# Kernel optimization log

Measured on AMD Instinct MI355X. Metric: run time of the kernel, lower is better.

The kernel has to match this reference:

```python
import jax, jax.numpy as jnp
import numpy as np

N = 50000      # nodes
E = 800000     # edges (before self loops)
H = 2          # attention heads
CH = 64        # per-head hidden channels
IN = 128       # input features
OUT = 64       # output channels
EPS = 1e-5     # batchnorm eps
SLOPE = 0.2    # LeakyReLU negative slope


def _gat_conv(x, src, dst, W, a_src, a_dst, b, concat):
    # x: [N, Fin]; W: [Fin, H*C]; a_src/a_dst: [H, C]
    n = x.shape[0]
    h = (x @ W).reshape(n, H, -1)                       # [N, H, C]
    al_s = (h * a_src).sum(-1)                          # [N, H]
    al_d = (h * a_dst).sum(-1)                          # [N, H]
    e = al_s[src] + al_d[dst]                           # [E, H]
    e = jnp.where(e > 0, e, SLOPE * e)                  # LeakyReLU
    # softmax over edges grouped by destination node
    m = jax.ops.segment_max(e, dst, num_segments=n)
    ex = jnp.exp(e - m[dst])
    den = jax.ops.segment_sum(ex, dst, num_segments=n)
    alpha = ex / (den[dst] + 1e-16)                     # [E, H]
    out = jax.ops.segment_sum(h[src] * alpha[:, :, None], dst, num_segments=n)
    out = out.reshape(n, -1) if concat else out.mean(axis=1)
    return out + b


def _batchnorm(x, g, be):
    mu = x.mean(axis=0)
    var = x.var(axis=0)  # biased, as torch BN uses in training
    return (x - mu) * jax.lax.rsqrt(var + EPS) * g + be


def setup_inputs() -> dict:
    key = jax.random.key(0)
    ks = jax.random.split(key, 18)
    s = 0.1
    inp = {
        "x": jax.random.normal(ks[0], (N, IN), jnp.float32),
        "edge_index": jax.random.randint(ks[1], (2, E), 0, N, jnp.int64),
        # layer 0: IN -> H*CH (concat)
        "W0": jax.random.normal(ks[2], (IN, H * CH), jnp.float32) * s,
        "a_src0": jax.random.normal(ks[3], (H, CH), jnp.float32) * s,
        "a_dst0": jax.random.normal(ks[4], (H, CH), jnp.float32) * s,
        "b0": jnp.zeros((H * CH,), jnp.float32),
        "g0": jnp.ones((H * CH,), jnp.float32),
        "be0": jnp.zeros((H * CH,), jnp.float32),
        # layer 1: H*CH -> H*CH (concat)
        "W1": jax.random.normal(ks[5], (H * CH, H * CH), jnp.float32) * s,
        "a_src1": jax.random.normal(ks[6], (H, CH), jnp.float32) * s,
        "a_dst1": jax.random.normal(ks[7], (H, CH), jnp.float32) * s,
        "b1": jnp.zeros((H * CH,), jnp.float32),
        "g1": jnp.ones((H * CH,), jnp.float32),
        "be1": jnp.zeros((H * CH,), jnp.float32),
        # layer 2: H*CH -> OUT, concat=False (mean over heads)
        "W2": jax.random.normal(ks[8], (H * CH, H * OUT), jnp.float32) * s,
        "a_src2": jax.random.normal(ks[9], (H, OUT), jnp.float32) * s,
        "a_dst2": jax.random.normal(ks[10], (H, OUT), jnp.float32) * s,
        "b2": jnp.zeros((OUT,), jnp.float32),
    }
    return inp


def reference(x, edge_index, W0, a_src0, a_dst0, b0, g0, be0,
              W1, a_src1, a_dst1, b1, g1, be1,
              W2, a_src2, a_dst2, b2):
    # add self loops (PyG GATConv default)
    loop = jnp.arange(N, dtype=edge_index.dtype)
    src = jnp.concatenate([edge_index[0], loop])
    dst = jnp.concatenate([edge_index[1], loop])

    h = _gat_conv(x, src, dst, W0, a_src0, a_dst0, b0, concat=True)
    h = jax.nn.relu(_batchnorm(h, g0, be0))
    # dropout: eval mode (identity)
    h = _gat_conv(h, src, dst, W1, a_src1, a_dst1, b1, concat=True)
    h = jax.nn.relu(_batchnorm(h, g1, be1))
    out = _gat_conv(h, src, dst, W2, a_src2, a_dst2, b2, concat=False)
    return out
```

## Files before the change

### kernel.cpp

```cpp
#include <hip/hip_runtime.h>


#define N_NODES 50000
#define N_EDGES 800000
#define ET (N_EDGES + N_NODES)
#define FDIM 128
#define SLOPE 0.2f
#define BN_EPS 1e-5f
#define SCAN_NB 196

typedef __attribute__((ext_vector_type(8))) short bf16x8;
typedef __attribute__((ext_vector_type(4))) float f32x4;
typedef __attribute__((ext_vector_type(8))) unsigned short u16x8;

__device__ __forceinline__ unsigned short f2bf(float f) {
  unsigned u = __float_as_uint(f);
  u = u + 0x7fffu + ((u >> 16) & 1u);
  return (unsigned short)(u >> 16);
}
__device__ __forceinline__ float bflo(unsigned p) { return __uint_as_float(p << 16); }
__device__ __forceinline__ float bfhi(unsigned p) { return __uint_as_float(p & 0xffff0000u); }


__global__ __launch_bounds__(256) void hist_rank(const int* __restrict__ dst,
                                                 int* __restrict__ counts,
                                                 int* __restrict__ rank) {
  int i = blockIdx.x * 256 + threadIdx.x;
  if (i >= ET) return;
  int d = (i < N_EDGES) ? dst[i] : i - N_EDGES;
  rank[i] = atomicAdd(&counts[d], 1);
}

__global__ __launch_bounds__(256) void scan_blk(const int* __restrict__ counts,
                                                int* __restrict__ rowptr,
                                                int* __restrict__ partials) {
  int i = blockIdx.x * 256 + threadIdx.x;
  int lane = threadIdx.x & 63, wv = threadIdx.x >> 6;
  int c = (i < N_NODES) ? counts[i] : 0;
  int v = c;
#pragma unroll
  for (int off = 1; off < 64; off <<= 1) {
    int u = __shfl_up(v, off);
    if (lane >= off) v += u;
  }
  __shared__ int wsum[4];
  if (lane == 63) wsum[wv] = v;
  __syncthreads();
  int add = 0;
  for (int w = 0; w < wv; ++w) add += wsum[w];
  if (i < N_NODES) rowptr[i] = v - c + add;
  if (threadIdx.x == 255) partials[blockIdx.x] = add + v;
}

__global__ __launch_bounds__(256) void scan_top(int* __restrict__ partials) {
  int t = threadIdx.x;
  int lane = t & 63, wv = t >> 6;
  int c = (t < SCAN_NB) ? partials[t] : 0;
  int v = c;
#pragma unroll
  for (int off = 1; off < 64; off <<= 1) {
    int u = __shfl_up(v, off);
    if (lane >= off) v += u;
  }
  __shared__ int wsum[4];
  if (lane == 63) wsum[wv] = v;
  __syncthreads();
  int add = 0;
  for (int w = 0; w < wv; ++w) add += wsum[w];
  if (t < SCAN_NB) partials[t] = v - c + add;
}

__global__ __launch_bounds__(256) void scan_fin(int* __restrict__ rowptr,
                                                const int* __restrict__ partials) {
  int i = blockIdx.x * 256 + threadIdx.x;
  if (i >= N_NODES) return;
  rowptr[i] += partials[blockIdx.x];
  if (i == 0) rowptr[N_NODES] = ET;
}

__global__ __launch_bounds__(256) void scatter_pos(const int* __restrict__ src,
                                                   const int* __restrict__ dst,
                                                   const int* __restrict__ rowptr,
                                                   const int* __restrict__ rank,
                                                   int* __restrict__ csr_src) {
  int i = blockIdx.x * 256 + threadIdx.x;
  if (i >= ET) return;
  int d, s;
  if (i < N_EDGES) { d = dst[i]; s = src[i]; } else { d = s = i - N_EDGES; }
  csr_src[rowptr[d] + rank[i]] = s;
}

__global__ __launch_bounds__(256) void repack_w(const float* __restrict__ W0,
                                                const float* __restrict__ W1,
                                                const float* __restrict__ W2,
                                                unsigned short* __restrict__ Wr) {
  int i = blockIdx.x * 256 + threadIdx.x;
  if (i >= 3 * 16384) return;
  int L = i >> 14, rem = i & 16383;
  int t  = rem >> 11;
  int ks = (rem >> 9) & 3;
  int ln = (rem >> 3) & 63;
  int j  = rem & 7;
  int k   = ks * 32 + (ln >> 4) * 8 + j;
  int col = t * 16 + (ln & 15);
  const float* W = (L == 0) ? W0 : ((L == 1) ? W1 : W2);
  Wr[i] = f2bf(W[k * 128 + col]);
}

__global__ __launch_bounds__(256) void gemm_mfma(const void* __restrict__ Xin,
                                                 const unsigned short* __restrict__ WrL,
                                                 const float* __restrict__ part,
                                                 const float* __restrict__ g,
                                                 const float* __restrict__ be,
                                                 const float* __restrict__ a_src,
                                                 const float* __restrict__ a_dst,
                                                 unsigned short* __restrict__ Hbf,
                                                 float* __restrict__ als,
                                                 float* __restrict__ ald,
                                                 int inBF) {
  __shared__ unsigned short lds[4][16][128];
  __shared__ float ls_scale[128], ls_shift[128];
  int lane = threadIdx.x & 63;
  int wv   = threadIdx.x >> 6;

  if (inBF) {
    int t = threadIdx.x;
    if (t < 128) {
      float s = 0.f, q = 0.f;
#pragma unroll
      for (int k = 0; k < 32; ++k) {
        s += part[k * 256 + t];
        q += part[k * 256 + 128 + t];
      }
      float mu  = s * (1.f / N_NODES);
      float var = q * (1.f / N_NODES) - mu * mu;
      float sc  = rsqrtf(var + BN_EPS) * g[t];
      ls_scale[t] = sc;
      ls_shift[t] = be[t] - mu * sc;
    }
    __syncthreads();
  }

  int row0 = blockIdx.x * 64 + wv * 16;
  int gidx = lane & 15;
  int quad = lane >> 4;
  int rA   = row0 + gidx;
  int rAc  = rA < N_NODES ? rA : N_NODES - 1;
  int koff = quad * 8;

  f32x4 acc[8] = {};
#pragma unroll
  for (int ks = 0; ks < 4; ++ks) {
    int cb = ks * 32 + koff;
    float xv[8];
    if (inBF) {
      const uint4* xr = (const uint4*)((const unsigned*)Xin + (size_t)rAc * 64 + (cb >> 1));
      uint4 xa = *xr;
      xv[0] = bflo(xa.x); xv[1] = bfhi(xa.x);
      xv[2] = bflo(xa.y); xv[3] = bfhi(xa.y);
      xv[4] = bflo(xa.z); xv[5] = bfhi(xa.z);
      xv[6] = bflo(xa.w); xv[7] = bfhi(xa.w);
    } else {
      const float4* xr = (const float4*)((const float*)Xin + (size_t)rAc * FDIM + cb);
      float4 xa = xr[0], xb = xr[1];
      xv[0] = xa.x; xv[1] = xa.y; xv[2] = xa.z; xv[3] = xa.w;
      xv[4] = xb.x; xv[5] = xb.y; xv[6] = xb.z; xv[7] = xb.w;
    }
    bf16x8 afrag;
    if (inBF) {
#pragma unroll
      for (int j = 0; j < 8; ++j) {
        int c = cb + j;
        float v = fmaf(xv[j], ls_scale[c], ls_shift[c]);
        v = v > 0.f ? v : 0.f;
        afrag[j] = (short)f2bf(v);
      }
    } else {
#pragma unroll
      for (int j = 0; j < 8; ++j) afrag[j] = (short)f2bf(xv[j]);
    }
#pragma unroll
    for (int t = 0; t < 8; ++t) {
      bf16x8 bfrag = *(const bf16x8*)(WrL + ((size_t)((t * 4 + ks) * 64 + lane)) * 8);
      acc[t] = __builtin_amdgcn_mfma_f32_16x16x32_bf16(afrag, bfrag, acc[t], 0, 0, 0);
    }
  }

  float vs[2][4] = {}, vd[2][4] = {};
#pragma unroll
  for (int t = 0; t < 8; ++t) {
    int col = t * 16 + gidx;
    float as = a_src[col], ad = a_dst[col];
    int hd = t >> 2;
#pragma unroll
    for (int r = 0; r < 4; ++r) {
      vs[hd][r] = fmaf(acc[t][r], as, vs[hd][r]);
      vd[hd][r] = fmaf(acc[t][r], ad, vd[hd][r]);
    }
  }
#pragma unroll
  for (int off = 1; off < 16; off <<= 1) {
#pragma unroll
    for (int hd = 0; hd < 2; ++hd)
#pragma unroll
      for (int r = 0; r < 4; ++r) {
        vs[hd][r] += __shfl_xor(vs[hd][r], off);
        vd[hd][r] += __shfl_xor(vd[hd][r], off);
      }
  }
  if (gidx == 0) {
#pragma unroll
    for (int r = 0; r < 4; ++r) {
      int row = row0 + quad * 4 + r;
      if (row < N_NODES) {
        als[row * 2 + 0] = vs[0][r]; als[row * 2 + 1] = vs[1][r];
        ald[row * 2 + 0] = vd[0][r]; ald[row * 2 + 1] = vd[1][r];
      }
    }
  }

#pragma unroll
  for (int t = 0; t < 8; ++t)
#pragma unroll
    for (int r = 0; r < 4; ++r)
      lds[wv][quad * 4 + r][t * 16 + gidx] = f2bf(acc[t][r]);
  __syncthreads();
#pragma unroll
  for (int it = 0; it < 4; ++it) {
    int rloc = it * 4 + quad;
    int row = row0 + rloc;
    if (row < N_NODES)
      *(u16x8*)(Hbf + (size_t)row * FDIM + gidx * 8) = *(u16x8*)&lds[wv][rloc][gidx * 8];
  }
}

__global__ __launch_bounds__(256) void fused_agg(const int* __restrict__ rowptr,
                                                 const int* __restrict__ csr_src,
                                                 const unsigned* __restrict__ H2,
                                                 const float* __restrict__ als,
                                                 const float* __restrict__ ald,
                                                 unsigned* __restrict__ Abf,
                                                 float* __restrict__ out,
                                                 const float* __restrict__ b2,
                                                 float* __restrict__ part,
                                                 int mode) {
  int lane = threadIdx.x & 63;
  bool hi = lane >= 32;
  int n = __builtin_amdgcn_readfirstlane((blockIdx.x * 256 + threadIdx.x) >> 6);
  int beg = rowptr[n], end = rowptr[n + 1];
  float2 adv = ((const float2*)ald)[n];
  float advh = hi ? adv.y : adv.x;

  int b0 = end - 4; if (b0 > beg) b0 = beg; if (b0 < 0) b0 = 0;
  int delta = beg - b0;
  int s0 = csr_src[b0], s1 = csr_src[b0 + 1], s2 = csr_src[b0 + 2], s3 = csr_src[b0 + 3];
  float2 A0 = ((const float2*)als)[s0];
  float2 A1 = ((const float2*)als)[s1];
  float2 A2 = ((const float2*)als)[s2];
  float2 A3 = ((const float2*)als)[s3];
  unsigned h0 = H2[(size_t)s0 * 64 + lane];
  unsigned h1 = H2[(size_t)s1 * 64 + lane];
  unsigned h2 = H2[(size_t)s2 * 64 + lane];
  unsigned h3 = H2[(size_t)s3 * 64 + lane];

  float l = 0.f, ox = 0.f, oy = 0.f;

#define STEP(AL, HH) { \
    float v_ = (hi ? AL.y : AL.x) + advh; \
    v_ = fmaxf(v_, SLOPE * v_); \
    float e_ = __expf(v_); \
    l += e_; \
    ox = fmaf(e_, bflo(HH), ox); \
    oy = fmaf(e_, bfhi(HH), oy); }

  int j = beg;
  for (; j + 4 <= end; j += 4) {
    int p = j + 4;
    int pp = p; if (pp > end - 4) pp = end - 4;
    int t0 = csr_src[pp], t1 = csr_src[pp + 1], t2 = csr_src[pp + 2], t3 = csr_src[pp + 3];
    float2 B0 = ((const float2*)als)[t0];
    float2 B1 = ((const float2*)als)[t1];
    float2 B2 = ((const float2*)als)[t2];
    float2 B3 = ((const float2*)als)[t3];
    unsigned g0 = H2[(size_t)t0 * 64 + lane];
    unsigned g1 = H2[(size_t)t1 * 64 + lane];
    unsigned g2 = H2[(size_t)t2 * 64 + lane];
    unsigned g3 = H2[(size_t)t3 * 64 + lane];

    STEP(A0, h0); STEP(A1, h1); STEP(A2, h2); STEP(A3, h3);

    delta = p - pp;
    A0 = B0; A1 = B1; A2 = B2; A3 = B3;
    h0 = g0; h1 = g1; h2 = g2; h3 = g3;
  }
  int rem = end - j;
  int hi_k = delta + rem;
  if (0 >= delta && 0 < hi_k) STEP(A0, h0);
  if (1 >= delta && 1 < hi_k) STEP(A1, h1);
  if (2 >= delta && 2 < hi_k) STEP(A2, h2);
  if (3 >= delta && 3 < hi_k) STEP(A3, h3);
#undef STEP

  float inv = 1.f / (l + 1e-16f);
  ox *= inv; oy *= inv;

  if (mode == 0) {
    unsigned pack = ((unsigned)f2bf(oy) << 16) | (unsigned)f2bf(ox);
    Abf[(size_t)n * 64 + lane] = pack;
    __shared__ float sh[4][4][64];
    int wv = threadIdx.x >> 6;
    sh[wv][0][lane] = ox;
    sh[wv][1][lane] = oy;
    sh[wv][2][lane] = ox * ox;
    sh[wv][3][lane] = oy * oy;
    __syncthreads();
    if (threadIdx.x < 64) {
      int t = threadIdx.x;
      float a0 = 0.f, a1 = 0.f, a2 = 0.f, a3 = 0.f;
#pragma unroll
      for (int w = 0; w < 4; ++w) {
        a0 += sh[w][0][t]; a1 += sh[w][1][t];
        a2 += sh[w][2][t]; a3 += sh[w][3][t];
      }
      float* slot = part + (blockIdx.x & 31) * 256;
      atomicAdd(&slot[2 * t],           a0);
      atomicAdd(&slot[2 * t + 1],       a1);
      atomicAdd(&slot[128 + 2 * t],     a2);
      atomicAdd(&slot[128 + 2 * t + 1], a3);
    }
  } else {
    float px = __shfl_xor(ox, 32);
    float py = __shfl_xor(oy, 32);
    if (lane < 32) {
      int c = lane * 2;
      float2 outv = {0.5f * (ox + px) + b2[c], 0.5f * (oy + py) + b2[c + 1]};
      *(float2*)(out + (size_t)n * 64 + c) = outv;
    }
  }
}

extern "C" void kernel_launch(void* const* d_in, const int* in_sizes, int n_in,
                              void* d_out, int out_size, void* d_ws, size_t ws_size,
                              hipStream_t stream) {
  const float* x  = (const float*)d_in[0];
  const int*   ei = (const int*)d_in[1];
  const int* src = ei;
  const int* dst = ei + N_EDGES;

  const float* W[3]    = {(const float*)d_in[2],  (const float*)d_in[8],  (const float*)d_in[14]};
  const float* asrc[3] = {(const float*)d_in[3],  (const float*)d_in[9],  (const float*)d_in[15]};
  const float* adst[3] = {(const float*)d_in[4],  (const float*)d_in[10], (const float*)d_in[16]};
  const float* g[2]    = {(const float*)d_in[6],  (const float*)d_in[12]};
  const float* be[2]   = {(const float*)d_in[7],  (const float*)d_in[13]};
  const float* b2      = (const float*)d_in[17];

  int*   counts   = (int*)d_ws;
  int*   rowptr   = counts + 50048;
  int*   partials = rowptr + 50048;
  int*   rank     = partials + 256;
  int*   csr_src  = rank + 850048;
  float* part     = (float*)(csr_src + 850048);
  float* als      = part + 8192;
  float* ald      = als + 100096;
  unsigned short* Wr  = (unsigned short*)(ald + 100096);
  unsigned short* Hbf = Wr + 3 * 16384;
  unsigned* Abf   = (unsigned*)(Hbf + (size_t)N_NODES * FDIM);

  hipMemsetAsync(counts, 0, (size_t)N_NODES * sizeof(int), stream);
  hist_rank<<<(ET + 255) / 256, 256, 0, stream>>>(dst, counts, rank);
  scan_blk<<<SCAN_NB, 256, 0, stream>>>(counts, rowptr, partials);
  scan_top<<<1, 256, 0, stream>>>(partials);
  scan_fin<<<SCAN_NB, 256, 0, stream>>>(rowptr, partials);
  scatter_pos<<<(ET + 255) / 256, 256, 0, stream>>>(src, dst, rowptr, rank, csr_src);
  repack_w<<<(3 * 16384 + 255) / 256, 256, 0, stream>>>(W[0], W[1], W[2], Wr);

  const int gemm_grid = (N_NODES + 63) / 64;
  const int agg_grid  = N_NODES * 64 / 256;

  for (int L = 0; L < 3; ++L) {
    const void* fin = (L == 0) ? (const void*)x : (const void*)Abf;
    int inBF = (L > 0);
    const float* gg = inBF ? g[L - 1]  : (const float*)nullptr;
    const float* bb = inBF ? be[L - 1] : (const float*)nullptr;
    gemm_mfma<<<gemm_grid, 256, 0, stream>>>(fin, Wr + (size_t)L * 16384, part, gg, bb,
                                             asrc[L], adst[L], Hbf, als, ald, inBF);
    if (L < 2)
      hipMemsetAsync(part, 0, 8192 * sizeof(float), stream);
    fused_agg<<<agg_grid, 256, 0, stream>>>(rowptr, csr_src, (const unsigned*)Hbf,
                                            als, ald, Abf, (float*)d_out, b2, part,
                                            (L == 2) ? 2 : 0);
  }
}
```

Baseline: 345.1 us.

## Fold attention vectors into GEMM, hoist BN finalize, deepen aggregation prefetch

Precomputes W·a_src and W·a_dst (scaled by log2e) as an extra 16-column MFMA tile, so attention logits come out of the GEMM instead of a per-tile dot product plus shuffle reduction. The aggregation switches to exp2f and widens the software-pipelined gather from 4 to 8 edges. Batchnorm statistics are finalized once in a small kernel instead of in every GEMM block. The scan_top kernel is removed by having each scan_fin block reduce the preceding partials itself. The trade-offs are one extra MFMA tile, lower logit precision because the folded vectors are rounded to bf16, and higher register pressure in the aggregation loop.

```diff
diff --git a/kernel.cpp b/kernel.cpp
--- a/kernel.cpp
+++ b/kernel.cpp
@@ -8,6 +8,8 @@
 #define SLOPE 0.2f
 #define BN_EPS 1e-5f
 #define SCAN_NB 196
+#define LOG2E 1.44269504088896340736f
+#define WSTRIDE 18432
 
 typedef __attribute__((ext_vector_type(8))) short bf16x8;
 typedef __attribute__((ext_vector_type(4))) float f32x4;
@@ -52,29 +54,20 @@
   if (threadIdx.x == 255) partials[blockIdx.x] = add + v;
 }
 
-__global__ __launch_bounds__(256) void scan_top(int* __restrict__ partials) {
-  int t = threadIdx.x;
-  int lane = t & 63, wv = t >> 6;
-  int c = (t < SCAN_NB) ? partials[t] : 0;
-  int v = c;
-#pragma unroll
-  for (int off = 1; off < 64; off <<= 1) {
-    int u = __shfl_up(v, off);
-    if (lane >= off) v += u;
-  }
-  __shared__ int wsum[4];
-  if (lane == 63) wsum[wv] = v;
-  __syncthreads();
-  int add = 0;
-  for (int w = 0; w < wv; ++w) add += wsum[w];
-  if (t < SCAN_NB) partials[t] = v - c + add;
-}
-
 __global__ __launch_bounds__(256) void scan_fin(int* __restrict__ rowptr,
                                                 const int* __restrict__ partials) {
-  int i = blockIdx.x * 256 + threadIdx.x;
-  if (i >= N_NODES) return;
-  rowptr[i] += partials[blockIdx.x];
+  __shared__ int sh[256];
+  int t = threadIdx.x;
+  sh[t] = (t < (int)blockIdx.x && t < SCAN_NB) ? partials[t] : 0;
+  __syncthreads();
+#pragma unroll
+  for (int off = 128; off > 0; off >>= 1) {
+    if (t < off) sh[t] += sh[t + off];
+    __syncthreads();
+  }
+  int base = sh[0];
+  int i = blockIdx.x * 256 + t;
+  if (i < N_NODES) rowptr[i] += base;
   if (i == 0) rowptr[N_NODES] = ET;
 }
 
@@ -93,27 +86,66 @@
 __global__ __launch_bounds__(256) void repack_w(const float* __restrict__ W0,
                                                 const float* __restrict__ W1,
                                                 const float* __restrict__ W2,
+                                                const float* __restrict__ as0,
+                                                const float* __restrict__ as1,
+                                                const float* __restrict__ as2,
+                                                const float* __restrict__ ad0,
+                                                const float* __restrict__ ad1,
+                                                const float* __restrict__ ad2,
                                                 unsigned short* __restrict__ Wr) {
   int i = blockIdx.x * 256 + threadIdx.x;
-  if (i >= 3 * 16384) return;
-  int L = i >> 14, rem = i & 16383;
+  if (i >= 3 * WSTRIDE) return;
+  int L = i / WSTRIDE, rem = i % WSTRIDE;
   int t  = rem >> 11;
   int ks = (rem >> 9) & 3;
   int ln = (rem >> 3) & 63;
   int j  = rem & 7;
-  int k   = ks * 32 + (ln >> 4) * 8 + j;
-  int col = t * 16 + (ln & 15);
+  int k  = ks * 32 + (ln >> 4) * 8 + j;
   const float* W = (L == 0) ? W0 : ((L == 1) ? W1 : W2);
-  Wr[i] = f2bf(W[k * 128 + col]);
+  float val;
+  if (t < 8) {
+    int col = t * 16 + (ln & 15);
+    val = W[k * 128 + col];
+  } else {
+    int cl = ln & 15;
+    if (cl < 4) {
+      int head = cl & 1;
+      const float* a = (cl < 2) ? ((L == 0) ? as0 : (L == 1) ? as1 : as2)
+                                : ((L == 0) ? ad0 : (L == 1) ? ad1 : ad2);
+      float s = 0.f;
+      const float* wrow = W + k * 128 + head * 64;
+      const float* ah = a + head * 64;
+#pragma unroll 8
+      for (int c = 0; c < 64; ++c) s = fmaf(wrow[c], ah[c], s);
+      val = s * LOG2E;
+    } else {
+      val = 0.f;
+    }
+  }
+  Wr[i] = f2bf(val);
+}
+
+__global__ __launch_bounds__(128) void bn_fin(const float* __restrict__ part,
+                                              const float* __restrict__ g,
+                                              const float* __restrict__ be,
+                                              float* __restrict__ lsbuf) {
+  int t = threadIdx.x;
+  float s = 0.f, q = 0.f;
+#pragma unroll
+  for (int k = 0; k < 32; ++k) {
+    s += part[k * 256 + t];
+    q += part[k * 256 + 128 + t];
+  }
+  float mu  = s * (1.f / N_NODES);
+  float var = q * (1.f / N_NODES) - mu * mu;
+  float sc  = rsqrtf(var + BN_EPS) * g[t];
+  lsbuf[t]       = sc;
+  lsbuf[128 + t] = be[t] - mu * sc;
 }
 
 __global__ __launch_bounds__(256) void gemm_mfma(const void* __restrict__ Xin,
                                                  const unsigned short* __restrict__ WrL,
-                                                 const float* __restrict__ part,
-                                                 const float* __restrict__ g,
-                                                 const float* __restrict__ be,
-                                                 const float* __restrict__ a_src,
-                                                 const float* __restrict__ a_dst,
+                                                 const float* __restrict__ lsbuf,
                                                  unsigned short* __restrict__ Hbf,
                                                  float* __restrict__ als,
                                                  float* __restrict__ ald,
@@ -126,17 +158,8 @@
   if (inBF) {
     int t = threadIdx.x;
     if (t < 128) {
-      float s = 0.f, q = 0.f;
-#pragma unroll
-      for (int k = 0; k < 32; ++k) {
-        s += part[k * 256 + t];
-        q += part[k * 256 + 128 + t];
-      }
-      float mu  = s * (1.f / N_NODES);
-      float var = q * (1.f / N_NODES) - mu * mu;
-      float sc  = rsqrtf(var + BN_EPS) * g[t];
-      ls_scale[t] = sc;
-      ls_shift[t] = be[t] - mu * sc;
+      ls_scale[t] = lsbuf[t];
+      ls_shift[t] = lsbuf[128 + t];
     }
     __syncthreads();
   }
@@ -148,7 +171,7 @@
   int rAc  = rA < N_NODES ? rA : N_NODES - 1;
   int koff = quad * 8;
 
-  f32x4 acc[8] = {};
+  f32x4 acc[9] = {};
 #pragma unroll
   for (int ks = 0; ks < 4; ++ks) {
     int cb = ks * 32 + koff;
@@ -180,42 +203,19 @@
       for (int j = 0; j < 8; ++j) afrag[j] = (short)f2bf(xv[j]);
     }
 #pragma unroll
-    for (int t = 0; t < 8; ++t) {
+    for (int t = 0; t < 9; ++t) {
       bf16x8 bfrag = *(const bf16x8*)(WrL + ((size_t)((t * 4 + ks) * 64 + lane)) * 8);
       acc[t] = __builtin_amdgcn_mfma_f32_16x16x32_bf16(afrag, bfrag, acc[t], 0, 0, 0);
     }
   }
 
-  float vs[2][4] = {}, vd[2][4] = {};
-#pragma unroll
-  for (int t = 0; t < 8; ++t) {
-    int col = t * 16 + gidx;
-    float as = a_src[col], ad = a_dst[col];
-    int hd = t >> 2;
-#pragma unroll
-    for (int r = 0; r < 4; ++r) {
-      vs[hd][r] = fmaf(acc[t][r], as, vs[hd][r]);
-      vd[hd][r] = fmaf(acc[t][r], ad, vd[hd][r]);
-    }
-  }
-#pragma unroll
-  for (int off = 1; off < 16; off <<= 1) {
-#pragma unroll
-    for (int hd = 0; hd < 2; ++hd)
-#pragma unroll
-      for (int r = 0; r < 4; ++r) {
-        vs[hd][r] += __shfl_xor(vs[hd][r], off);
-        vd[hd][r] += __shfl_xor(vd[hd][r], off);
-      }
-  }
-  if (gidx == 0) {
+  if (gidx < 4) {
+    float* dp = (gidx < 2) ? als : ald;
+    int hd = gidx & 1;
 #pragma unroll
     for (int r = 0; r < 4; ++r) {
       int row = row0 + quad * 4 + r;
-      if (row < N_NODES) {
-        als[row * 2 + 0] = vs[0][r]; als[row * 2 + 1] = vs[1][r];
-        ald[row * 2 + 0] = vd[0][r]; ald[row * 2 + 1] = vd[1][r];
-      }
+      if (row < N_NODES) dp[row * 2 + hd] = acc[8][r];
     }
   }
 
@@ -251,54 +251,53 @@
   float2 adv = ((const float2*)ald)[n];
   float advh = hi ? adv.y : adv.x;
 
-  int b0 = end - 4; if (b0 > beg) b0 = beg; if (b0 < 0) b0 = 0;
+  int b0 = end - 8; if (b0 > beg) b0 = beg; if (b0 < 0) b0 = 0;
   int delta = beg - b0;
-  int s0 = csr_src[b0], s1 = csr_src[b0 + 1], s2 = csr_src[b0 + 2], s3 = csr_src[b0 + 3];
-  float2 A0 = ((const float2*)als)[s0];
-  float2 A1 = ((const float2*)als)[s1];
-  float2 A2 = ((const float2*)als)[s2];
-  float2 A3 = ((const float2*)als)[s3];
-  unsigned h0 = H2[(size_t)s0 * 64 + lane];
-  unsigned h1 = H2[(size_t)s1 * 64 + lane];
-  unsigned h2 = H2[(size_t)s2 * 64 + lane];
-  unsigned h3 = H2[(size_t)s3 * 64 + lane];
+  int sa[8]; float2 aa[8]; unsigned ha[8];
+#pragma unroll
+  for (int i = 0; i < 8; ++i) sa[i] = csr_src[b0 + i];
+#pragma unroll
+  for (int i = 0; i < 8; ++i) {
+    aa[i] = ((const float2*)als)[sa[i]];
+    ha[i] = H2[(size_t)sa[i] * 64 + lane];
+  }
 
   float l = 0.f, ox = 0.f, oy = 0.f;
 
-#define STEP(AL, HH) { \
-    float v_ = (hi ? AL.y : AL.x) + advh; \
+#define STEP(i) { \
+    float v_ = (hi ? aa[i].y : aa[i].x) + advh; \
     v_ = fmaxf(v_, SLOPE * v_); \
-    float e_ = __expf(v_); \
+    float e_ = exp2f(v_); \
     l += e_; \
-    ox = fmaf(e_, bflo(HH), ox); \
-    oy = fmaf(e_, bfhi(HH), oy); }
+    ox = fmaf(e_, bflo(ha[i]), ox); \
+    oy = fmaf(e_, bfhi(ha[i]), oy); }
 
   int j = beg;
-  for (; j + 4 <= end; j += 4) {
-    int p = j + 4;
-    int pp = p; if (pp > end - 4) pp = end - 4;
-    int t0 = csr_src[pp], t1 = csr_src[pp + 1], t2 = csr_src[pp + 2], t3 = csr_src[pp + 3];
-    float2 B0 = ((const float2*)als)[t0];
-    float2 B1 = ((const float2*)als)[t1];
-    float2 B2 = ((const float2*)als)[t2];
-    float2 B3 = ((const float2*)als)[t3];
-    unsigned g0 = H2[(size_t)t0 * 64 + lane];
-    unsigned g1 = H2[(size_t)t1 * 64 + lane];
-    unsigned g2 = H2[(size_t)t2 * 64 + lane];
-    unsigned g3 = H2[(size_t)t3 * 64 + lane];
-
-    STEP(A0, h0); STEP(A1, h1); STEP(A2, h2); STEP(A3, h3);
-
-    delta = p - pp;
-    A0 = B0; A1 = B1; A2 = B2; A3 = B3;
-    h0 = g0; h1 = g1; h2 = g2; h3 = g3;
+  for (; j + 8 <= end; j += 8) {
+    int pp = j + 8; if (pp > end - 8) pp = end - 8;
+    int sn[8]; float2 an[8]; unsigned hn[8];
+#pragma unroll
+    for (int i = 0; i < 8; ++i) sn[i] = csr_src[pp + i];
+#pragma unroll
+    for (int i = 0; i < 8; ++i) {
+      an[i] = ((const float2*)als)[sn[i]];
+      hn[i] = H2[(size_t)sn[i] * 64 + lane];
+    }
+    STEP(0); STEP(1); STEP(2); STEP(3); STEP(4); STEP(5); STEP(6); STEP(7);
+    delta = j + 8 - pp;
+#pragma unroll
+    for (int i = 0; i < 8; ++i) { aa[i] = an[i]; ha[i] = hn[i]; }
   }
   int rem = end - j;
-  int hi_k = delta + rem;
-  if (0 >= delta && 0 < hi_k) STEP(A0, h0);
-  if (1 >= delta && 1 < hi_k) STEP(A1, h1);
-  if (2 >= delta && 2 < hi_k) STEP(A2, h2);
-  if (3 >= delta && 3 < hi_k) STEP(A3, h3);
+  int hik = delta + rem;
+  if (0 >= delta && 0 < hik) STEP(0);
+  if (1 >= delta && 1 < hik) STEP(1);
+  if (2 >= delta && 2 < hik) STEP(2);
+  if (3 >= delta && 3 < hik) STEP(3);
+  if (4 >= delta && 4 < hik) STEP(4);
+  if (5 >= delta && 5 < hik) STEP(5);
+  if (6 >= delta && 6 < hik) STEP(6);
+  if (7 >= delta && 7 < hik) STEP(7);
 #undef STEP
 
   float inv = 1.f / (l + 1e-16f);
@@ -360,19 +359,20 @@
   int*   rank     = partials + 256;
   int*   csr_src  = rank + 850048;
   float* part     = (float*)(csr_src + 850048);
-  float* als      = part + 8192;
+  float* lsbuf    = part + 8192;
+  float* als      = lsbuf + 256;
   float* ald      = als + 100096;
   unsigned short* Wr  = (unsigned short*)(ald + 100096);
-  unsigned short* Hbf = Wr + 3 * 16384;
+  unsigned short* Hbf = Wr + 3 * WSTRIDE + 128;
   unsigned* Abf   = (unsigned*)(Hbf + (size_t)N_NODES * FDIM);
 
   hipMemsetAsync(counts, 0, (size_t)N_NODES * sizeof(int), stream);
   hist_rank<<<(ET + 255) / 256, 256, 0, stream>>>(dst, counts, rank);
   scan_blk<<<SCAN_NB, 256, 0, stream>>>(counts, rowptr, partials);
-  scan_top<<<1, 256, 0, stream>>>(partials);
   scan_fin<<<SCAN_NB, 256, 0, stream>>>(rowptr, partials);
   scatter_pos<<<(ET + 255) / 256, 256, 0, stream>>>(src, dst, rowptr, rank, csr_src);
-  repack_w<<<(3 * 16384 + 255) / 256, 256, 0, stream>>>(W[0], W[1], W[2], Wr);
+  repack_w<<<(3 * WSTRIDE + 255) / 256, 256, 0, stream>>>(
+      W[0], W[1], W[2], asrc[0], asrc[1], asrc[2], adst[0], adst[1], adst[2], Wr);
 
   const int gemm_grid = (N_NODES + 63) / 64;
   const int agg_grid  = N_NODES * 64 / 256;
@@ -380,14 +380,14 @@
   for (int L = 0; L < 3; ++L) {
     const void* fin = (L == 0) ? (const void*)x : (const void*)Abf;
     int inBF = (L > 0);
-    const float* gg = inBF ? g[L - 1]  : (const float*)nullptr;
-    const float* bb = inBF ? be[L - 1] : (const float*)nullptr;
-    gemm_mfma<<<gemm_grid, 256, 0, stream>>>(fin, Wr + (size_t)L * 16384, part, gg, bb,
-                                             asrc[L], adst[L], Hbf, als, ald, inBF);
+    gemm_mfma<<<gemm_grid, 256, 0, stream>>>(fin, Wr + (size_t)L * WSTRIDE, lsbuf,
+                                             Hbf, als, ald, inBF);
     if (L < 2)
       hipMemsetAsync(part, 0, 8192 * sizeof(float), stream);
     fused_agg<<<agg_grid, 256, 0, stream>>>(rowptr, csr_src, (const unsigned*)Hbf,
                                             als, ald, Abf, (float*)d_out, b2, part,
                                             (L == 2) ? 2 : 0);
-  }
-}
+    if (L < 2)
+      bn_fin<<<1, 128, 0, stream>>>(part, g[L], be[L], lsbuf);
+  }
+}
```

After: 339.8 us. Within noise of the previous version (-1.5%).
